# Optimization experiments

Measured on AMD Instinct MI355X. Metric: run time of the kernel, lower is better.

The kernel has to match this reference:

```python
import jax, jax.numpy as jnp
import numpy as np

NUM_HEADS = 16
HIDDEN = 1024
B, S = 2, 2048


def setup_inputs() -> dict:
    key = jax.random.key(0)
    ks = jax.random.split(key, 14)
    D = HIDDEN
    scale = 1.0 / np.sqrt(D)
    inp = {
        "query": jax.random.normal(ks[0], (B, S, D), jnp.float32),
        "key_in": jax.random.normal(ks[1], (B, S, D), jnp.float32),
        "value": jax.random.normal(ks[2], (B, S, D), jnp.float32),
        "group_prob": jax.random.uniform(ks[3], (B, S, S), jnp.float32),
        "mask": jax.random.randint(ks[4], (B, S, S), 0, 2, jnp.int32),
        "wq_k": jax.random.normal(ks[5], (D, D), jnp.float32) * scale,
        "wq_b": jnp.zeros((D,), jnp.float32),
        "wk_k": jax.random.normal(ks[6], (D, D), jnp.float32) * scale,
        "wk_b": jnp.zeros((D,), jnp.float32),
        "wv_k": jax.random.normal(ks[7], (D, D), jnp.float32) * scale,
        "wv_b": jnp.zeros((D,), jnp.float32),
        "wo_k": jax.random.normal(ks[8], (D, D), jnp.float32) * scale,
        "wo_b": jnp.zeros((D,), jnp.float32),
    }
    return inp


def _split_heads(x, H):
    b, s, d = x.shape
    return x.reshape(b, s, H, d // H).transpose(0, 2, 1, 3)  # (B,H,S,dh)


def reference(query, key_in, value, group_prob, mask,
              wq_k, wq_b, wk_k, wk_b, wv_k, wv_b, wo_k, wo_b):
    H = NUM_HEADS
    dh = query.shape[-1] // H
    q = _split_heads(query @ wq_k + wq_b, H)
    k = _split_heads(key_in @ wk_k + wk_b, H)
    v = _split_heads(value @ wv_k + wv_b, H)
    # scaled dot-product logits (B,H,Sq,Sk)
    logits = jnp.einsum('bhqd,bhkd->bhqk', q, k) / jnp.sqrt(jnp.asarray(dh, q.dtype))
    neg = (1.0 - mask.astype(q.dtype)) * -1e9
    logits = logits + neg[:, None, :, :]
    attn = jax.nn.softmax(logits, axis=-1)
    # Tree Transformer modulation: post-softmax elementwise scale by group_prob
    attn = attn * group_prob[:, None, :, :]
    out = jnp.einsum('bhqk,bhkd->bhqd', attn, v)
    out = out.transpose(0, 2, 1, 3).reshape(query.shape[0], -1, H * dh)
    return out @ wo_k + wo_b
```

## Files before the change

### kernel.cpp

```cpp
#include <hip/hip_runtime.h>
#include <hip/hip_bf16.h>
#include <stdint.h>

#define B_ 2
#define S_ 2048
#define D_ 1024
#define H_ 16
#define DH 64

typedef __attribute__((ext_vector_type(4))) float f32x4;
typedef __attribute__((ext_vector_type(8))) short s16x8;
typedef __attribute__((ext_vector_type(4))) short s16x4;

__device__ inline short f2bf(float f) {
  union { float f; unsigned u; } v; v.f = f;
  unsigned r = (v.u + 0x7fffu + ((v.u >> 16) & 1u)) >> 16;
  return (short)r;
}

__device__ inline float bfbits_lo(unsigned u) {
  union { unsigned x; float f; } v; v.x = u << 16; return v.f;
}
__device__ inline float bfbits_hi(unsigned u) {
  union { unsigned x; float f; } v; v.x = u & 0xffff0000u; return v.f;
}

__device__ inline float exp2v(float x) {
  float r; asm("v_exp_f32 %0, %1" : "=v"(r) : "v"(x)); return r;
}
__device__ inline unsigned cvtpk(float a, float b) {
  unsigned r; asm("v_cvt_pk_bf16_f32 %0, %1, %2" : "=v"(r) : "v"(a), "v"(b));
  return r;
}

__global__ __launch_bounds__(256) void cvt3_f32_bf16(const float* __restrict__ a,
                                                     const float* __restrict__ b,
                                                     const float* __restrict__ c,
                                                     short* oa, short* ob, short* oc,
                                                     int n) {
  int z = blockIdx.y;
  const float* in = z == 0 ? a : (z == 1 ? b : c);
  short* out = z == 0 ? oa : (z == 1 ? ob : oc);
  int i = (blockIdx.x * 256 + threadIdx.x) * 4;
  if (i < n) {
    float4 v = *(const float4*)(in + i);
    s16x4 o;
    o.x = f2bf(v.x); o.y = f2bf(v.y); o.z = f2bf(v.z); o.w = f2bf(v.w);
    *(s16x4*)(out + i) = o;
  }
}

__global__ __launch_bounds__(256) void fuse_mgp(const int* __restrict__ mask,
                                                const float* __restrict__ gp,
                                                short* __restrict__ mgp, int n) {
  int i = (blockIdx.x * 256 + threadIdx.x) * 4;
  if (i < n) {
    int4 m = *(const int4*)(mask + i);
    float4 g = *(const float4*)(gp + i);
    short b0 = f2bf(g.x); if (!b0) b0 = (short)0x0080;
    short b1 = f2bf(g.y); if (!b1) b1 = (short)0x0080;
    short b2 = f2bf(g.z); if (!b2) b2 = (short)0x0080;
    short b3 = f2bf(g.w); if (!b3) b3 = (short)0x0080;
    s16x4 o;
    o.x = m.x ? b0 : 0;
    o.y = m.y ? b1 : 0;
    o.z = m.z ? b2 : 0;
    o.w = m.w ? b3 : 0;
    *(s16x4*)(mgp + i) = o;
  }
}

__global__ __launch_bounds__(256) void transpose_cvt4(
    const float* __restrict__ i0, const float* __restrict__ i1,
    const float* __restrict__ i2, const float* __restrict__ i3,
    short* o0, short* o1, short* o2, short* o3) {
  int z = blockIdx.z;
  const float* in = z == 0 ? i0 : (z == 1 ? i1 : (z == 2 ? i2 : i3));
  short* out = z == 0 ? o0 : (z == 1 ? o1 : (z == 2 ? o2 : o3));
  __shared__ float tile[32][33];
  int bx = blockIdx.x, by = blockIdx.y;
  int x = bx * 32 + threadIdx.x;
#pragma unroll
  for (int i = 0; i < 32; i += 8) {
    int y = by * 32 + threadIdx.y + i;
    tile[threadIdx.y + i][threadIdx.x] = in[(size_t)y * D_ + x];
  }
  __syncthreads();
  int ox = by * 32 + threadIdx.x;
#pragma unroll
  for (int i = 0; i < 32; i += 8) {
    int oy = bx * 32 + threadIdx.y + i;
    out[(size_t)oy * D_ + ox] = f2bf(tile[threadIdx.x][threadIdx.y + i]);
  }
}

__global__ __launch_bounds__(256) void transpose_v(const short* __restrict__ vp,
                                                   short* __restrict__ vt) {
  __shared__ __align__(16) short t[64 * 72];
  int tid = threadIdx.x;
  int bh = blockIdx.y, b = bh >> 4, h = bh & 15;
  int s0 = blockIdx.x * 64;
  int r = tid >> 2, cc = tid & 3;
  const short* src = vp + ((size_t)(b * S_ + s0 + r)) * D_ + h * DH + cc * 16;
  s16x8 a = *(const s16x8*)src;
  s16x8 bb = *(const s16x8*)(src + 8);
  int pc = (cc ^ (r >> 4)) * 16;
  *(s16x8*)&t[r * 72 + pc] = a;
  *(s16x8*)&t[r * 72 + pc + 8] = bb;
  __syncthreads();
  int d = tid >> 2, sc = (tid & 3) * 16;
  s16x8 o0, o1;
#pragma unroll
  for (int j = 0; j < 8; ++j) {
    int row = sc + j;
    o0[j] = t[row * 72 + ((d >> 4) ^ (row >> 4)) * 16 + (d & 15)];
    int row2 = sc + 8 + j;
    o1[j] = t[row2 * 72 + ((d >> 4) ^ (row2 >> 4)) * 16 + (d & 15)];
  }
  short* dst = vt + ((size_t)(b * H_ + h) * DH + d) * S_ + s0 + sc;
  *(s16x8*)dst = o0;
  *(s16x8*)(dst + 8) = o1;
}

__device__ inline void gload_lds16(const void* g, void* l) {
  __builtin_amdgcn_global_load_lds(
      (const __attribute__((address_space(1))) unsigned*)g,
      (__attribute__((address_space(3))) unsigned*)l, 16, 0, 0);
}

#define BM 128
#define BN 128
#define BK 32

__global__ __launch_bounds__(256) void gemm_bt3(
    const short* __restrict__ A0, const short* __restrict__ A1, const short* __restrict__ A2,
    const short* __restrict__ Bt0, const short* __restrict__ Bt1, const short* __restrict__ Bt2,
    const float* __restrict__ bs0, const float* __restrict__ bs1, const float* __restrict__ bs2,
    void* C0, void* C1, void* C2,
    int M, int N, int K, int f32out, float os0, float os1, float os2) {
  int z = blockIdx.y;
  const short* A = z == 0 ? A0 : (z == 1 ? A1 : A2);
  const short* Bt = z == 0 ? Bt0 : (z == 1 ? Bt1 : Bt2);
  const float* bias = z == 0 ? bs0 : (z == 1 ? bs1 : bs2);
  void* C = z == 0 ? C0 : (z == 1 ? C1 : C2);
  float oscale = z == 0 ? os0 : (z == 1 ? os1 : os2);

  __shared__ __align__(16) short As[BM * BK];
  __shared__ __align__(16) short Bs[BN * BK];
  int tid = threadIdx.x;
  int lane = tid & 63, wave = tid >> 6;
  int l15 = lane & 15, l4 = lane >> 4;
  int ntn = N / BN;
  int bm = blockIdx.x / ntn, bn = blockIdx.x % ntn;
  int row0 = bm * BM, col0 = bn * BN;
  int wm = (wave >> 1) * 64, wn = (wave & 1) * 64;

  f32x4 acc[4][4] = {};

  for (int k0 = 0; k0 < K; k0 += BK) {
    __syncthreads();
#pragma unroll
    for (int it = 0; it < 2; ++it) {
      int ch = it * 256 + tid;
      int r = ch >> 2, c = (ch & 3) * 8;
      int ldsbase = (it * 256 + wave * 64) * 8;
      gload_lds16(A + (size_t)(row0 + r) * K + k0 + c, &As[ldsbase]);
      gload_lds16(Bt + (size_t)(col0 + r) * K + k0 + c, &Bs[ldsbase]);
    }
    __syncthreads();
    s16x8 af[4], bf[4];
#pragma unroll
    for (int mf = 0; mf < 4; ++mf)
      af[mf] = *(const s16x8*)&As[(wm + mf * 16 + l15) * BK + l4 * 8];
#pragma unroll
    for (int nf = 0; nf < 4; ++nf)
      bf[nf] = *(const s16x8*)&Bs[(wn + nf * 16 + l15) * BK + l4 * 8];
#pragma unroll
    for (int mf = 0; mf < 4; ++mf)
#pragma unroll
      for (int nf = 0; nf < 4; ++nf)
        acc[mf][nf] = __builtin_amdgcn_mfma_f32_16x16x32_bf16(af[mf], bf[nf],
                                                              acc[mf][nf], 0, 0, 0);
  }

#pragma unroll
  for (int nf = 0; nf < 4; ++nf) {
    int gcol = col0 + wn + nf * 16 + l15;
    float bv = bias[gcol];
#pragma unroll
    for (int mf = 0; mf < 4; ++mf) {
#pragma unroll
      for (int r = 0; r < 4; ++r) {
        int grow = row0 + wm + mf * 16 + l4 * 4 + r;
        float v = (acc[mf][nf][r] + bv) * oscale;
        if (f32out)
          ((float*)C)[(size_t)grow * N + gcol] = v;
        else
          ((short*)C)[(size_t)grow * N + gcol] = f2bf(v);
      }
    }
  }
}

#define QB 128
#define NB 64
#define NTILES (S_ / NB)
#define M0_SHIFT 12.0f

__global__ __launch_bounds__(256, 3) void attn_fused(const short* __restrict__ Qp,
                                                     const short* __restrict__ Kp,
                                                     const short* __restrict__ VT,
                                                     const short* __restrict__ MGP,
                                                     short* __restrict__ ctx) {
  __shared__ __align__(16) short Ks[2][64 * 64];
  __shared__ __align__(16) short Vs[2][64 * 64];
  __shared__ __align__(16) short Ps[4][32 * 64];

  int tid = threadIdx.x, lane = tid & 63, wave = tid >> 6;
  int l15 = lane & 15, l4 = lane >> 4;
  int q0 = blockIdx.x * QB;
  int bh = blockIdx.y;
  int b = bh >> 4, h = bh & 15;
  int wq = wave * 32;

  const short* Qbase = Qp + (size_t)b * S_ * D_ + (size_t)h * DH;
  const short* Kbase = Kp + (size_t)b * S_ * D_ + (size_t)h * DH;
  const short* Vbase = VT + (size_t)(b * H_ + h) * DH * S_;
  const short* Mrow0 = MGP + (size_t)b * S_ * S_ + (size_t)(q0 + wq + l15) * S_ + l4 * 4;
  const short* Mrow1 = Mrow0 + (size_t)16 * S_;

  int i0 = tid, i1 = 256 + tid;
  int r0 = i0 >> 3, c0 = (i0 & 7) ^ (r0 & 7);
  int r1 = i1 >> 3, c1 = (i1 & 7) ^ (r1 & 7);
  int ldsA = wave * 512;
  int ldsB = 2048 + wave * 512;

#define STAGE(kv0, buf)                                                       \
  do {                                                                        \
    gload_lds16(Kbase + (size_t)((kv0) + r0) * D_ + c0 * 8, &Ks[buf][ldsA]);  \
    gload_lds16(Kbase + (size_t)((kv0) + r1) * D_ + c1 * 8, &Ks[buf][ldsB]);  \
    gload_lds16(Vbase + (size_t)r0 * S_ + (kv0) + c0 * 8, &Vs[buf][ldsA]);    \
    gload_lds16(Vbase + (size_t)r1 * S_ + (kv0) + c1 * 8, &Vs[buf][ldsB]);    \
  } while (0)

  s16x8 qf[2][2];
#pragma unroll
  for (int mf = 0; mf < 2; ++mf)
#pragma unroll
    for (int ks = 0; ks < 2; ++ks)
      qf[mf][ks] = *(const s16x8*)(Qbase + (size_t)(q0 + wq + mf * 16 + l15) * D_ +
                                   ks * 32 + l4 * 8);

  float lsum[2] = {0.f, 0.f};
  f32x4 oacc[2][4] = {};

  STAGE(0, 0);

  int q7 = l15 & 7;
  short* Pw = &Ps[wave][0];
  int prow[2] = {l15 * 64, (16 + l15) * 64};

  for (int t = 0; t < NTILES; ++t) {
    int buf = t & 1;
    int kvt = t * NB;

    uint2 g2[2][4];
#pragma unroll
    for (int nf = 0; nf < 4; ++nf) {
      g2[0][nf] = *(const uint2*)(Mrow0 + kvt + nf * 16);
      g2[1][nf] = *(const uint2*)(Mrow1 + kvt + nf * 16);
    }
    __builtin_amdgcn_sched_barrier(0);
    if (t + 1 < NTILES) {
      STAGE((t + 1) * NB, buf ^ 1);
      __builtin_amdgcn_sched_barrier(0);
      asm volatile("s_waitcnt vmcnt(12)" ::: "memory");
    } else {
      __builtin_amdgcn_sched_barrier(0);
      asm volatile("s_waitcnt vmcnt(8)" ::: "memory");
    }
    __builtin_amdgcn_s_barrier();
    __builtin_amdgcn_sched_barrier(0);

    f32x4 sacc[2][4] = {};
#pragma unroll
    for (int nf = 0; nf < 4; ++nf) {
      int R = nf * 16 + l15;
#pragma unroll
      for (int ks = 0; ks < 2; ++ks) {
        s16x8 kf = *(const s16x8*)&Ks[buf][R * 64 + (((ks * 4 + l4) ^ q7) * 8)];
#pragma unroll
        for (int mf = 0; mf < 2; ++mf)
          sacc[mf][nf] = __builtin_amdgcn_mfma_f32_16x16x32_bf16(kf, qf[mf][ks],
                                                                 sacc[mf][nf], 0, 0, 0);
      }
    }

    if (t + 1 < NTILES)
      asm volatile("s_waitcnt vmcnt(4)" ::: "memory");
    else
      asm volatile("s_waitcnt vmcnt(0)" ::: "memory");
    __builtin_amdgcn_sched_barrier(0);

#pragma unroll
    for (int mf = 0; mf < 2; ++mf) {
#pragma unroll
      for (int nf = 0; nf < 4; ++nf) {
        float gv0 = bfbits_lo(g2[mf][nf].x), gv1 = bfbits_hi(g2[mf][nf].x);
        float gv2 = bfbits_lo(g2[mf][nf].y), gv3 = bfbits_hi(g2[mf][nf].y);
        float e0 = exp2v(sacc[mf][nf][0] - M0_SHIFT);
        float e1 = exp2v(sacc[mf][nf][1] - M0_SHIFT);
        float e2 = exp2v(sacc[mf][nf][2] - M0_SHIFT);
        float e3 = exp2v(sacc[mf][nf][3] - M0_SHIFT);
        lsum[mf] += (gv0 != 0.f) ? e0 : 0.f;
        lsum[mf] += (gv1 != 0.f) ? e1 : 0.f;
        lsum[mf] += (gv2 != 0.f) ? e2 : 0.f;
        lsum[mf] += (gv3 != 0.f) ? e3 : 0.f;
        uint2 wp;
        wp.x = cvtpk(e0 * gv0, e1 * gv1);
        wp.y = cvtpk(e2 * gv2, e3 * gv3);
        int gr = ((nf * 2 + (l4 >> 1)) ^ q7) * 8 + (l4 & 1) * 4;
        *(uint2*)&Pw[prow[mf] + gr] = wp;
      }
    }

#pragma unroll
    for (int ks = 0; ks < 2; ++ks) {
      s16x8 pa[2];
#pragma unroll
      for (int mf = 0; mf < 2; ++mf)
        pa[mf] = *(const s16x8*)&Pw[prow[mf] + (((ks * 4 + l4) ^ q7) * 8)];
#pragma unroll
      for (int df = 0; df < 4; ++df) {
        s16x8 vf = *(const s16x8*)&Vs[buf][(df * 16 + l15) * 64 +
                                           (((ks * 4 + l4) ^ q7) * 8)];
#pragma unroll
        for (int mf = 0; mf < 2; ++mf)
          oacc[mf][df] = __builtin_amdgcn_mfma_f32_16x16x32_bf16(vf, pa[mf],
                                                                 oacc[mf][df], 0, 0, 0);
      }
    }

    asm volatile("s_waitcnt lgkmcnt(0)" ::: "memory");
    __builtin_amdgcn_s_barrier();
  }
#undef STAGE

#pragma unroll
  for (int mf = 0; mf < 2; ++mf) {
    float ls = lsum[mf];
    ls += __shfl_xor(ls, 16);
    ls += __shfl_xor(ls, 32);
    float inv = 1.f / ls;
    short* crow = ctx + ((size_t)(b * S_ + q0 + wq + mf * 16 + l15)) * D_ + h * DH;
#pragma unroll
    for (int df = 0; df < 4; ++df) {
      uint2 o;
      o.x = cvtpk(oacc[mf][df][0] * inv, oacc[mf][df][1] * inv);
      o.y = cvtpk(oacc[mf][df][2] * inv, oacc[mf][df][3] * inv);
      *(uint2*)(crow + df * 16 + l4 * 4) = o;
    }
  }
}

extern "C" void kernel_launch(void* const* d_in, const int* in_sizes, int n_in,
                              void* d_out, int out_size, void* d_ws, size_t ws_size,
                              hipStream_t stream) {
  const float* query = (const float*)d_in[0];
  const float* key_in = (const float*)d_in[1];
  const float* value = (const float*)d_in[2];
  const float* group_prob = (const float*)d_in[3];
  const int* mask = (const int*)d_in[4];
  const float* wq_k = (const float*)d_in[5];
  const float* wq_b = (const float*)d_in[6];
  const float* wk_k = (const float*)d_in[7];
  const float* wk_b = (const float*)d_in[8];
  const float* wv_k = (const float*)d_in[9];
  const float* wv_b = (const float*)d_in[10];
  const float* wo_k = (const float*)d_in[11];
  const float* wo_b = (const float*)d_in[12];
  float* out = (float*)d_out;

  short* ws = (short*)d_ws;
  const size_t NT = (size_t)B_ * S_ * D_;
  short* qbf = ws;
  short* kbf = qbf + NT;
  short* vbf = kbf + NT;
  short* wqt = vbf + NT;
  short* wkt = wqt + (size_t)D_ * D_;
  short* wvt = wkt + (size_t)D_ * D_;
  short* wot = wvt + (size_t)D_ * D_;
  short* qp = wot + (size_t)D_ * D_;
  short* kp = qp + NT;
  short* vp = kp + NT;
  short* ctx = vp + NT;
  short* mgp = ws;
  short* vt = vbf;

  int nblk = (int)(NT / 4 / 256);
  cvt3_f32_bf16<<<dim3(nblk, 3), 256, 0, stream>>>(query, key_in, value,
                                                   qbf, kbf, vbf, (int)NT);

  dim3 tb(32, 8);
  transpose_cvt4<<<dim3(D_ / 32, D_ / 32, 4), tb, 0, stream>>>(
      wq_k, wk_k, wv_k, wo_k, wqt, wkt, wvt, wot);

  int M = B_ * S_;
  int gblocks = (M / BM) * (D_ / BN);
  const float QSCALE = 0.125f * 1.4426950408889634f;
  gemm_bt3<<<dim3(gblocks, 3), 256, 0, stream>>>(
      qbf, kbf, vbf, wqt, wkt, wvt, wq_b, wk_b, wv_b, qp, kp, vp,
      M, D_, D_, 0, QSCALE, 1.0f, 1.0f);

  int nmg = B_ * S_ * S_;
  fuse_mgp<<<nmg / 4 / 256, 256, 0, stream>>>(mask, group_prob, mgp, nmg);
  transpose_v<<<dim3(S_ / 64, B_ * H_), 256, 0, stream>>>(vp, vt);

  dim3 ag(S_ / QB, B_ * H_);
  attn_fused<<<ag, 256, 0, stream>>>(qp, kp, vt, mgp, ctx);

  gemm_bt3<<<dim3(gblocks, 1), 256, 0, stream>>>(
      ctx, ctx, ctx, wot, wot, wot, wo_b, wo_b, wo_b, out, out, out,
      M, D_, D_, 1, 1.0f, 1.0f, 1.0f);
}
```

Baseline: 188.0 us.

## Merge mask prep and V transpose, swizzle GEMM blocks, hoist exp with setprio

```diff
diff --git a/kernel.cpp b/kernel.cpp
--- a/kernel.cpp
+++ b/kernel.cpp
@@ -50,11 +50,41 @@
   }
 }
 
-__global__ __launch_bounds__(256) void fuse_mgp(const int* __restrict__ mask,
-                                                const float* __restrict__ gp,
-                                                short* __restrict__ mgp, int n) {
-  int i = (blockIdx.x * 256 + threadIdx.x) * 4;
-  if (i < n) {
+__global__ __launch_bounds__(256) void transpose_cvt4(
+    const float* __restrict__ i0, const float* __restrict__ i1,
+    const float* __restrict__ i2, const float* __restrict__ i3,
+    short* o0, short* o1, short* o2, short* o3) {
+  int z = blockIdx.z;
+  const float* in = z == 0 ? i0 : (z == 1 ? i1 : (z == 2 ? i2 : i3));
+  short* out = z == 0 ? o0 : (z == 1 ? o1 : (z == 2 ? o2 : o3));
+  __shared__ float tile[32][33];
+  int bx = blockIdx.x, by = blockIdx.y;
+  int x = bx * 32 + threadIdx.x;
+#pragma unroll
+  for (int i = 0; i < 32; i += 8) {
+    int y = by * 32 + threadIdx.y + i;
+    tile[threadIdx.y + i][threadIdx.x] = in[(size_t)y * D_ + x];
+  }
+  __syncthreads();
+  int ox = by * 32 + threadIdx.x;
+#pragma unroll
+  for (int i = 0; i < 32; i += 8) {
+    int oy = bx * 32 + threadIdx.y + i;
+    out[(size_t)oy * D_ + ox] = f2bf(tile[threadIdx.x][threadIdx.y + i]);
+  }
+}
+
+#define FUSE_BLK ((B_ * S_ * S_) / 1024)
+__global__ __launch_bounds__(256) void prep_attn(const int* __restrict__ mask,
+                                                 const float* __restrict__ gp,
+                                                 short* __restrict__ mgp,
+                                                 const short* __restrict__ vp,
+                                                 short* __restrict__ vt) {
+  __shared__ __align__(16) short t[64 * 72];
+  int bid = blockIdx.x;
+  int tid = threadIdx.x;
+  if (bid < FUSE_BLK) {
+    int i = (bid * 256 + tid) * 4;
     int4 m = *(const int4*)(mask + i);
     float4 g = *(const float4*)(gp + i);
     short b0 = f2bf(g.x); if (!b0) b0 = (short)0x0080;
@@ -67,59 +97,31 @@
     o.z = m.z ? b2 : 0;
     o.w = m.w ? b3 : 0;
     *(s16x4*)(mgp + i) = o;
-  }
-}
-
-__global__ __launch_bounds__(256) void transpose_cvt4(
-    const float* __restrict__ i0, const float* __restrict__ i1,
-    const float* __restrict__ i2, const float* __restrict__ i3,
-    short* o0, short* o1, short* o2, short* o3) {
-  int z = blockIdx.z;
-  const float* in = z == 0 ? i0 : (z == 1 ? i1 : (z == 2 ? i2 : i3));
-  short* out = z == 0 ? o0 : (z == 1 ? o1 : (z == 2 ? o2 : o3));
-  __shared__ float tile[32][33];
-  int bx = blockIdx.x, by = blockIdx.y;
-  int x = bx * 32 + threadIdx.x;
-#pragma unroll
-  for (int i = 0; i < 32; i += 8) {
-    int y = by * 32 + threadIdx.y + i;
-    tile[threadIdx.y + i][threadIdx.x] = in[(size_t)y * D_ + x];
-  }
-  __syncthreads();
-  int ox = by * 32 + threadIdx.x;
-#pragma unroll
-  for (int i = 0; i < 32; i += 8) {
-    int oy = bx * 32 + threadIdx.y + i;
-    out[(size_t)oy * D_ + ox] = f2bf(tile[threadIdx.x][threadIdx.y + i]);
-  }
-}
-
-__global__ __launch_bounds__(256) void transpose_v(const short* __restrict__ vp,
-                                                   short* __restrict__ vt) {
-  __shared__ __align__(16) short t[64 * 72];
-  int tid = threadIdx.x;
-  int bh = blockIdx.y, b = bh >> 4, h = bh & 15;
-  int s0 = blockIdx.x * 64;
-  int r = tid >> 2, cc = tid & 3;
-  const short* src = vp + ((size_t)(b * S_ + s0 + r)) * D_ + h * DH + cc * 16;
-  s16x8 a = *(const s16x8*)src;
-  s16x8 bb = *(const s16x8*)(src + 8);
-  int pc = (cc ^ (r >> 4)) * 16;
-  *(s16x8*)&t[r * 72 + pc] = a;
-  *(s16x8*)&t[r * 72 + pc + 8] = bb;
-  __syncthreads();
-  int d = tid >> 2, sc = (tid & 3) * 16;
-  s16x8 o0, o1;
-#pragma unroll
-  for (int j = 0; j < 8; ++j) {
-    int row = sc + j;
-    o0[j] = t[row * 72 + ((d >> 4) ^ (row >> 4)) * 16 + (d & 15)];
-    int row2 = sc + 8 + j;
-    o1[j] = t[row2 * 72 + ((d >> 4) ^ (row2 >> 4)) * 16 + (d & 15)];
-  }
-  short* dst = vt + ((size_t)(b * H_ + h) * DH + d) * S_ + s0 + sc;
-  *(s16x8*)dst = o0;
-  *(s16x8*)(dst + 8) = o1;
+  } else {
+    int l = bid - FUSE_BLK;
+    int s0 = (l & 31) * 64;
+    int bh = l >> 5, b = bh >> 4, h = bh & 15;
+    int r = tid >> 2, cc = tid & 3;
+    const short* src = vp + ((size_t)(b * S_ + s0 + r)) * D_ + h * DH + cc * 16;
+    s16x8 a = *(const s16x8*)src;
+    s16x8 bb = *(const s16x8*)(src + 8);
+    int pc = (cc ^ (r >> 4)) * 16;
+    *(s16x8*)&t[r * 72 + pc] = a;
+    *(s16x8*)&t[r * 72 + pc + 8] = bb;
+    __syncthreads();
+    int d = tid >> 2, sc = (tid & 3) * 16;
+    s16x8 o0, o1;
+#pragma unroll
+    for (int j = 0; j < 8; ++j) {
+      int row = sc + j;
+      o0[j] = t[row * 72 + ((d >> 4) ^ (row >> 4)) * 16 + (d & 15)];
+      int row2 = sc + 8 + j;
+      o1[j] = t[row2 * 72 + ((d >> 4) ^ (row2 >> 4)) * 16 + (d & 15)];
+    }
+    short* dst = vt + ((size_t)(b * H_ + h) * DH + d) * S_ + s0 + sc;
+    *(s16x8*)dst = o0;
+    *(s16x8*)(dst + 8) = o1;
+  }
 }
 
 __device__ inline void gload_lds16(const void* g, void* l) {
@@ -151,7 +153,9 @@
   int lane = tid & 63, wave = tid >> 6;
   int l15 = lane & 15, l4 = lane >> 4;
   int ntn = N / BN;
-  int bm = blockIdx.x / ntn, bn = blockIdx.x % ntn;
+  int bid = blockIdx.x;
+  bid = ((bid & 7) << 5) | (bid >> 3);
+  int bm = bid / ntn, bn = bid % ntn;
   int row0 = bm * BM, col0 = bn * BN;
   int wm = (wave >> 1) * 64, wn = (wave & 1) * 64;
 
@@ -283,6 +287,7 @@
     __builtin_amdgcn_sched_barrier(0);
 
     f32x4 sacc[2][4] = {};
+    __builtin_amdgcn_s_setprio(1);
 #pragma unroll
     for (int nf = 0; nf < 4; ++nf) {
       int R = nf * 16 + l15;
@@ -295,6 +300,16 @@
                                                                  sacc[mf][nf], 0, 0, 0);
       }
     }
+    __builtin_amdgcn_s_setprio(0);
+
+    float ee[2][4][4];
+#pragma unroll
+    for (int mf = 0; mf < 2; ++mf)
+#pragma unroll
+      for (int nf = 0; nf < 4; ++nf)
+#pragma unroll
+        for (int r = 0; r < 4; ++r)
+          ee[mf][nf][r] = exp2v(sacc[mf][nf][r] - M0_SHIFT);
 
     if (t + 1 < NTILES)
       asm volatile("s_waitcnt vmcnt(4)" ::: "memory");
@@ -308,10 +323,8 @@
       for (int nf = 0; nf < 4; ++nf) {
         float gv0 = bfbits_lo(g2[mf][nf].x), gv1 = bfbits_hi(g2[mf][nf].x);
         float gv2 = bfbits_lo(g2[mf][nf].y), gv3 = bfbits_hi(g2[mf][nf].y);
-        float e0 = exp2v(sacc[mf][nf][0] - M0_SHIFT);
-        float e1 = exp2v(sacc[mf][nf][1] - M0_SHIFT);
-        float e2 = exp2v(sacc[mf][nf][2] - M0_SHIFT);
-        float e3 = exp2v(sacc[mf][nf][3] - M0_SHIFT);
+        float e0 = ee[mf][nf][0], e1 = ee[mf][nf][1];
+        float e2 = ee[mf][nf][2], e3 = ee[mf][nf][3];
         lsum[mf] += (gv0 != 0.f) ? e0 : 0.f;
         lsum[mf] += (gv1 != 0.f) ? e1 : 0.f;
         lsum[mf] += (gv2 != 0.f) ? e2 : 0.f;
@@ -324,6 +337,7 @@
       }
     }
 
+    __builtin_amdgcn_s_setprio(1);
 #pragma unroll
     for (int ks = 0; ks < 2; ++ks) {
       s16x8 pa[2];
@@ -340,6 +354,7 @@
                                                                  oacc[mf][df], 0, 0, 0);
       }
     }
+    __builtin_amdgcn_s_setprio(0);
 
     asm volatile("s_waitcnt lgkmcnt(0)" ::: "memory");
     __builtin_amdgcn_s_barrier();
@@ -412,9 +427,8 @@
       qbf, kbf, vbf, wqt, wkt, wvt, wq_b, wk_b, wv_b, qp, kp, vp,
       M, D_, D_, 0, QSCALE, 1.0f, 1.0f);
 
-  int nmg = B_ * S_ * S_;
-  fuse_mgp<<<nmg / 4 / 256, 256, 0, stream>>>(mask, group_prob, mgp, nmg);
-  transpose_v<<<dim3(S_ / 64, B_ * H_), 256, 0, stream>>>(vp, vt);
+  prep_attn<<<FUSE_BLK + (S_ / 64) * B_ * H_, 256, 0, stream>>>(
+      mask, group_prob, mgp, vp, vt);
 
   dim3 ag(S_ / QB, B_ * H_);
   attn_fused<<<ag, 256, 0, stream>>>(qp, kp, vt, mgp, ctx);
```

Measured after the change: 181.0 us. 1.04x faster.
